# Performance work log

Measured on AMD Instinct MI355X. Metric: run time of the kernel, lower is better.

The kernel has to match this reference:

```python
import jax, jax.numpy as jnp
import numpy as np

B, N, L, D, H, DH = 1, 512, 256, 256, 8, 32  # batch, n_seqs, length, d_msa, heads, d_hidden
EPS = 1e-5


def setup_inputs() -> dict:
    key = jax.random.key(0)
    ks = jax.random.split(key, 3)
    msa = jax.random.normal(ks[0], (B, N, L, D), dtype=jnp.float32)
    # xavier-uniform-ish scale for (H*DH, D) linear weights
    lim = float(np.sqrt(6.0 / (D + H * DH)))
    Wq = jax.random.uniform(ks[1], (H * DH, D), minval=-lim, maxval=lim, dtype=jnp.float32)
    Wk = jax.random.uniform(ks[2], (H * DH, D), minval=-lim, maxval=lim, dtype=jnp.float32)
    return {
        "msa": msa,
        "Wq": Wq,
        "bq": jnp.zeros((H * DH,), jnp.float32),
        "Wk": Wk,
        "bk": jnp.zeros((H * DH,), jnp.float32),
        "ln_gamma": jnp.ones((D,), jnp.float32),
        "ln_beta": jnp.zeros((D,), jnp.float32),
        "stride": 0,
    }


def reference(msa, Wq, bq, Wk, bk, ln_gamma, ln_beta, stride):
    # stride only controls chunking in the original (no math effect); ignored.
    def ln(x):
        m = jnp.mean(x, axis=-1, keepdims=True)
        v = jnp.mean((x - m) ** 2, axis=-1, keepdims=True)
        return (x - m) * jax.lax.rsqrt(v + EPS) * ln_gamma + ln_beta

    scale = 1.0 / np.sqrt(DH)
    b, n, l = msa.shape[:3]
    # query from target (first) sequence: (B, L, H, DH)
    q = (ln(msa[:, 0]) @ Wq.T + bq).reshape(b, l, H, DH) * scale
    # keys from all sequences: (B, N, L, H, DH)
    k = (ln(msa) @ Wk.T + bk).reshape(b, n, l, H, DH)
    # attention logits over the sequence axis N: (B, N, L, H)
    logits = jnp.einsum("blhd,bnlhd->bnlh", q, k)
    attn = jax.nn.softmax(logits, axis=1)
    # dropout is identity in eval mode
    return attn[..., None]  # (B, N, L, H, 1)
```

## Files before the change

kernel.cpp:

```cpp
#include <hip/hip_runtime.h>
#include <hip/hip_bf16.h>
#include <cstdint>

#define LL 256
#define NN 512
#define DD 256
#define HH 8
#define EPSF 1e-5f
#define WGS 264
#define TS  264

typedef __attribute__((ext_vector_type(8))) __bf16 bf16x8;
typedef __attribute__((ext_vector_type(4))) __bf16 bf16x4;
typedef __attribute__((ext_vector_type(4))) float f32x4;

static __device__ __forceinline__ void lb_sync() {
    __builtin_amdgcn_sched_barrier(0);
    asm volatile("s_waitcnt lgkmcnt(0)" ::: "memory");
    __builtin_amdgcn_s_barrier();
    __builtin_amdgcn_sched_barrier(0);
}

static __device__ __forceinline__ void loadg(
    const float* __restrict__ msa, int l, int wave, int lane, int t, float4 (&buf)[16])
{
    #pragma unroll
    for (int r = 0; r < 16; ++r)
        buf[r] = *((const float4*)(msa + ((size_t)(t * 128 + wave * 16 + r) * LL + l) * DD) + lane);
}

static __device__ __forceinline__ void dswcvt(
    const float4 (&buf)[16], __bf16* tile, int wave, int lane)
{
    #pragma unroll
    for (int r = 0; r < 16; ++r) {
        float4 u = buf[r];
        bf16x4 b;
        b[0] = (__bf16)u.x; b[1] = (__bf16)u.y; b[2] = (__bf16)u.z; b[3] = (__bf16)u.w;
        *(bf16x4*)(tile + (wave * 16 + r) * TS + lane * 4) = b;
    }
}

static __device__ __forceinline__ void compute_t(
    int g, const __bf16* tile, const bf16x8 (&bfr)[8], int wave, int col, int kb,
    float* logits, float* sS, float* sQ)
{
    f32x4 ha = {0.f, 0.f, 0.f, 0.f}, ga = {0.f, 0.f, 0.f, 0.f};
    const __bf16* arow = tile + (wave * 16 + col) * TS;
    #pragma unroll
    for (int ks = 0; ks < 8; ++ks) {
        bf16x8 a = *(const bf16x8*)(arow + ks * 32 + kb * 8);
        ha = __builtin_amdgcn_mfma_f32_16x16x32_bf16(a, bfr[ks], ha, 0, 0, 0);
        ga = __builtin_amdgcn_mfma_f32_16x16x32_bf16(a, a,       ga, 0, 0, 0);
    }
    const int nb = g * 128 + wave * 16;
    #pragma unroll
    for (int i = 0; i < 4; ++i) {
        int n = nb + (kb << 2) + i;
        if (col < HH)       logits[col * NN + n] = ha[i];
        else if (col == HH) sS[n] = ha[i];
    }
    if (kb == (col >> 2)) sQ[nb + col] = ga[col & 3];
}

__global__ __launch_bounds__(512, 2) void k_fused(
    const float* __restrict__ msa, const float* __restrict__ Wq,
    const float* __restrict__ bq, const float* __restrict__ Wk,
    const float* __restrict__ gamma, const float* __restrict__ beta,
    float* __restrict__ out)
{
    const int l = blockIdx.x;
    const int tid = threadIdx.x, wave = tid >> 6, lane = tid & 63;
    const int col = lane & 15, kb = lane >> 4;

    __shared__ __align__(16) __bf16 tile[128 * TS];
    __shared__ __align__(16) __bf16 WgL[16 * WGS];
    __shared__ __align__(16) float logits[HH * NN];
    __shared__ __align__(16) float sS[NN];
    __shared__ __align__(16) float sQ[NN];
    __shared__ float lnx[DD];
    __shared__ float qv[DD];
    __shared__ float red[8];
    __shared__ float stats[16];
    __shared__ float Gs[HH];

    float4 P[16], Q[16];
    loadg(msa, l, wave, lane, 0, P);
    loadg(msa, l, wave, lane, 1, Q);

    {
        float x0 = (tid < DD) ? msa[(size_t)l * DD + tid] : 0.f;
        float s = x0, ss = x0 * x0;
        #pragma unroll
        for (int m = 32; m >= 1; m >>= 1) { s += __shfl_xor(s, m); ss += __shfl_xor(ss, m); }
        if (tid < DD && lane == 0) { red[wave * 2] = s; red[wave * 2 + 1] = ss; }
        lb_sync();
        if (tid < DD) {
            float sm = red[0] + red[2] + red[4] + red[6];
            float sq = red[1] + red[3] + red[5] + red[7];
            float mean = sm * (1.f / DD);
            float var  = sq * (1.f / DD) - mean * mean;
            float rs   = rsqrtf(var + EPSF);
            lnx[tid] = (x0 - mean) * rs * gamma[tid] + beta[tid];
        }
        lb_sync();
        const int r = tid & 255, hf = tid >> 8;
        float acc = 0.f;
        {
            const float4* wr = (const float4*)(Wq + (size_t)r * DD) + hf * 32;
            const float* lx = lnx + hf * 128;
            #pragma unroll 4
            for (int j = 0; j < 32; ++j) {
                float4 w4 = wr[j];
                acc += lx[4*j] * w4.x + lx[4*j+1] * w4.y + lx[4*j+2] * w4.z + lx[4*j+3] * w4.w;
            }
        }
        if (hf == 0) qv[r] = acc;
        lb_sync();
        if (hf == 1) qv[r] = (qv[r] + acc + bq[r]) * 0.17677669529663687f;
        lb_sync();
        const int c = tid & 255, h0 = (tid >> 8) * 4;
        const float gm = gamma[c];
        #pragma unroll
        for (int hi = 0; hi < 4; ++hi) {
            int h = h0 + hi;
            float a = 0.f;
            const float* wk = Wk + ((size_t)h * 32) * DD + c;
            #pragma unroll 8
            for (int d = 0; d < 32; ++d)
                a += qv[h * 32 + d] * wk[(size_t)d * DD];
            WgL[h * WGS + c] = (__bf16)(gm * a);
        }
        if (tid < DD) {
            WgL[8 * WGS + tid] = (__bf16)1.0f;
        } else {
            const int c2 = tid - 256;
            #pragma unroll
            for (int h = 9; h < 16; ++h) WgL[h * WGS + c2] = (__bf16)0.0f;
        }
        lb_sync();
        if (wave < HH) {
            float gsum = 0.f;
            #pragma unroll
            for (int i = 0; i < 4; ++i) gsum += (float)WgL[wave * WGS + lane * 4 + i];
            #pragma unroll
            for (int m = 32; m >= 1; m >>= 1) gsum += __shfl_xor(gsum, m);
            if (lane == 0) Gs[wave] = gsum;
        }
        lb_sync();
    }

    bf16x8 bfr[8];
    #pragma unroll
    for (int ks = 0; ks < 8; ++ks)
        bfr[ks] = *(const bf16x8*)&WgL[col * WGS + ks * 32 + kb * 8];

    dswcvt(P, tile, wave, lane);  loadg(msa, l, wave, lane, 2, P);  lb_sync();
    compute_t(0, tile, bfr, wave, col, kb, logits, sS, sQ);         lb_sync();
    dswcvt(Q, tile, wave, lane);  loadg(msa, l, wave, lane, 3, Q);  lb_sync();
    compute_t(1, tile, bfr, wave, col, kb, logits, sS, sQ);         lb_sync();
    dswcvt(P, tile, wave, lane);                                    lb_sync();
    compute_t(2, tile, bfr, wave, col, kb, logits, sS, sQ);         lb_sync();
    dswcvt(Q, tile, wave, lane);                                    lb_sync();
    compute_t(3, tile, bfr, wave, col, kb, logits, sS, sQ);         lb_sync();

    {
        const int h = wave;
        const float Gh = Gs[h];
        const float* lp = logits + h * NN;
        float4 ra = ((const float4*)lp)[lane * 2];
        float4 rb = ((const float4*)lp)[lane * 2 + 1];
        float4 sa = ((const float4*)sS)[lane * 2];
        float4 sb = ((const float4*)sS)[lane * 2 + 1];
        float4 qa = ((const float4*)sQ)[lane * 2];
        float4 qb = ((const float4*)sQ)[lane * 2 + 1];
        float raw[8] = {ra.x, ra.y, ra.z, ra.w, rb.x, rb.y, rb.z, rb.w};
        float sv[8]  = {sa.x, sa.y, sa.z, sa.w, sb.x, sb.y, sb.z, sb.w};
        float qv2[8] = {qa.x, qa.y, qa.z, qa.w, qb.x, qb.y, qb.z, qb.w};
        float adj[8];
        #pragma unroll
        for (int i = 0; i < 8; ++i) {
            float mean = sv[i] * (1.f / DD);
            float var  = qv2[i] * (1.f / DD) - mean * mean;
            float rs   = rsqrtf(var + EPSF);
            adj[i] = rs * (raw[i] - mean * Gh);
        }
        float mx = adj[0];
        #pragma unroll
        for (int i = 1; i < 8; ++i) mx = fmaxf(mx, adj[i]);
        #pragma unroll
        for (int m = 32; m >= 1; m >>= 1) mx = fmaxf(mx, __shfl_xor(mx, m));
        float sm = 0.f;
        #pragma unroll
        for (int i = 0; i < 8; ++i) sm += __expf(adj[i] - mx);
        #pragma unroll
        for (int m = 32; m >= 1; m >>= 1) sm += __shfl_xor(sm, m);
        if (lane == 0) { stats[wave] = mx; stats[8 + wave] = 1.f / sm; }
    }
    lb_sync();

    {
        const int n = tid;
        float s = sS[n], q2 = sQ[n];
        float mean = s * (1.f / DD);
        float var  = q2 * (1.f / DD) - mean * mean;
        float rs   = rsqrtf(var + EPSF);
        float o[8];
        #pragma unroll
        for (int h = 0; h < HH; ++h) {
            float adj = rs * (logits[h * NN + n] - mean * Gs[h]);
            o[h] = __expf(adj - stats[h]) * stats[8 + h];
        }
        float* op = out + (size_t)n * LL * HH + (size_t)l * HH;
        float4 p0 = {o[0], o[1], o[2], o[3]};
        float4 p1 = {o[4], o[5], o[6], o[7]};
        *(float4*)(op)     = p0;
        *(float4*)(op + 4) = p1;
    }
}

extern "C" void kernel_launch(void* const* d_in, const int* in_sizes, int n_in,
                              void* d_out, int out_size, void* d_ws, size_t ws_size,
                              hipStream_t stream) {
    (void)in_sizes; (void)n_in; (void)out_size; (void)d_ws; (void)ws_size;
    const float* msa   = (const float*)d_in[0];
    const float* Wq    = (const float*)d_in[1];
    const float* bq    = (const float*)d_in[2];
    const float* Wk    = (const float*)d_in[3];
    const float* gamma = (const float*)d_in[5];
    const float* beta  = (const float*)d_in[6];
    k_fused<<<dim3(LL), dim3(512), 0, stream>>>(msa, Wq, bq, Wk, gamma, beta, (float*)d_out);
}
```

Baseline: 44.77 us.

## Warp-specialize producer waves with async global-to-LDS double-buffered fp32 tiles

Replaces the register-staged load/convert/store pipeline with four producer waves that issue global_load_lds copies straight into two fp32 LDS tile buffers of 64 rows each. Four consumer waves convert to bf16 on the fly and run the MFMAs, with vmcnt waits and barriers handing off each buffer. To fit LDS, the WgL, lnx, qv and red scratch buffers are aliased into the logits buffer, and the Gs reduction moves after the bfr loads. The aim is to free the large register prefetch buffers and overlap memory traffic with compute. In exchange, half the waves no longer do MFMA, barriers run every step, and the larger LDS footprint limits residency to one block per CU.

```diff
diff --git a/kernel.cpp b/kernel.cpp
--- a/kernel.cpp
+++ b/kernel.cpp
@@ -8,10 +8,10 @@
 #define HH 8
 #define EPSF 1e-5f
 #define WGS 264
-#define TS  264
+#define TROWF 260
+#define TILEF (64 * TROWF)
 
 typedef __attribute__((ext_vector_type(8))) __bf16 bf16x8;
-typedef __attribute__((ext_vector_type(4))) __bf16 bf16x4;
 typedef __attribute__((ext_vector_type(4))) float f32x4;
 
 static __device__ __forceinline__ void lb_sync() {
@@ -21,49 +21,20 @@
     __builtin_amdgcn_sched_barrier(0);
 }
 
-static __device__ __forceinline__ void loadg(
-    const float* __restrict__ msa, int l, int wave, int lane, int t, float4 (&buf)[16])
+static __device__ __forceinline__ void stage16(
+    const float* __restrict__ msa, int l, int n0, float* ldsrow0, int lane)
 {
     #pragma unroll
-    for (int r = 0; r < 16; ++r)
-        buf[r] = *((const float4*)(msa + ((size_t)(t * 128 + wave * 16 + r) * LL + l) * DD) + lane);
-}
-
-static __device__ __forceinline__ void dswcvt(
-    const float4 (&buf)[16], __bf16* tile, int wave, int lane)
-{
-    #pragma unroll
-    for (int r = 0; r < 16; ++r) {
-        float4 u = buf[r];
-        bf16x4 b;
-        b[0] = (__bf16)u.x; b[1] = (__bf16)u.y; b[2] = (__bf16)u.z; b[3] = (__bf16)u.w;
-        *(bf16x4*)(tile + (wave * 16 + r) * TS + lane * 4) = b;
-    }
-}
-
-static __device__ __forceinline__ void compute_t(
-    int g, const __bf16* tile, const bf16x8 (&bfr)[8], int wave, int col, int kb,
-    float* logits, float* sS, float* sQ)
-{
-    f32x4 ha = {0.f, 0.f, 0.f, 0.f}, ga = {0.f, 0.f, 0.f, 0.f};
-    const __bf16* arow = tile + (wave * 16 + col) * TS;
-    #pragma unroll
-    for (int ks = 0; ks < 8; ++ks) {
-        bf16x8 a = *(const bf16x8*)(arow + ks * 32 + kb * 8);
-        ha = __builtin_amdgcn_mfma_f32_16x16x32_bf16(a, bfr[ks], ha, 0, 0, 0);
-        ga = __builtin_amdgcn_mfma_f32_16x16x32_bf16(a, a,       ga, 0, 0, 0);
-    }
-    const int nb = g * 128 + wave * 16;
-    #pragma unroll
-    for (int i = 0; i < 4; ++i) {
-        int n = nb + (kb << 2) + i;
-        if (col < HH)       logits[col * NN + n] = ha[i];
-        else if (col == HH) sS[n] = ha[i];
-    }
-    if (kb == (col >> 2)) sQ[nb + col] = ga[col & 3];
-}
-
-__global__ __launch_bounds__(512, 2) void k_fused(
+    for (int i = 0; i < 16; ++i) {
+        const float* g = msa + ((size_t)(n0 + i) * LL + l) * DD + lane * 4;
+        __builtin_amdgcn_global_load_lds(
+            (const __attribute__((address_space(1))) void*)g,
+            (__attribute__((address_space(3))) void*)(ldsrow0 + (size_t)i * TROWF),
+            16, 0, 0);
+    }
+}
+
+__global__ __launch_bounds__(512) void k_fused(
     const float* __restrict__ msa, const float* __restrict__ Wq,
     const float* __restrict__ bq, const float* __restrict__ Wk,
     const float* __restrict__ gamma, const float* __restrict__ beta,
@@ -73,20 +44,24 @@
     const int tid = threadIdx.x, wave = tid >> 6, lane = tid & 63;
     const int col = lane & 15, kb = lane >> 4;
 
-    __shared__ __align__(16) __bf16 tile[128 * TS];
-    __shared__ __align__(16) __bf16 WgL[16 * WGS];
-    __shared__ __align__(16) float logits[HH * NN];
+    __shared__ __align__(16) float TileF[2 * TILEF];
+    __shared__ __align__(16) float logitsBuf[HH * NN];
     __shared__ __align__(16) float sS[NN];
     __shared__ __align__(16) float sQ[NN];
-    __shared__ float lnx[DD];
-    __shared__ float qv[DD];
-    __shared__ float red[8];
     __shared__ float stats[16];
     __shared__ float Gs[HH];
 
-    float4 P[16], Q[16];
-    loadg(msa, l, wave, lane, 0, P);
-    loadg(msa, l, wave, lane, 1, Q);
+    __bf16* WgL = (__bf16*)logitsBuf;
+    float*  lnx = logitsBuf + 2112;
+    float*  qv  = lnx + 256;
+    float*  red = qv + 256;
+    float*  logits = logitsBuf;
+
+    if (wave >= 4) {
+        const int pid = wave - 4;
+        stage16(msa, l, 0 * 64 + pid * 16, TileF + 0 * TILEF + pid * 16 * TROWF, lane);
+        stage16(msa, l, 1 * 64 + pid * 16, TileF + 1 * TILEF + pid * 16 * TROWF, lane);
+    }
 
     {
         float x0 = (tid < DD) ? msa[(size_t)l * DD + tid] : 0.f;
@@ -139,30 +114,59 @@
             for (int h = 9; h < 16; ++h) WgL[h * WGS + c2] = (__bf16)0.0f;
         }
         lb_sync();
-        if (wave < HH) {
-            float gsum = 0.f;
-            #pragma unroll
-            for (int i = 0; i < 4; ++i) gsum += (float)WgL[wave * WGS + lane * 4 + i];
-            #pragma unroll
-            for (int m = 32; m >= 1; m >>= 1) gsum += __shfl_xor(gsum, m);
-            if (lane == 0) Gs[wave] = gsum;
-        }
-        lb_sync();
     }
 
     bf16x8 bfr[8];
     #pragma unroll
     for (int ks = 0; ks < 8; ++ks)
         bfr[ks] = *(const bf16x8*)&WgL[col * WGS + ks * 32 + kb * 8];
-
-    dswcvt(P, tile, wave, lane);  loadg(msa, l, wave, lane, 2, P);  lb_sync();
-    compute_t(0, tile, bfr, wave, col, kb, logits, sS, sQ);         lb_sync();
-    dswcvt(Q, tile, wave, lane);  loadg(msa, l, wave, lane, 3, Q);  lb_sync();
-    compute_t(1, tile, bfr, wave, col, kb, logits, sS, sQ);         lb_sync();
-    dswcvt(P, tile, wave, lane);                                    lb_sync();
-    compute_t(2, tile, bfr, wave, col, kb, logits, sS, sQ);         lb_sync();
-    dswcvt(Q, tile, wave, lane);                                    lb_sync();
-    compute_t(3, tile, bfr, wave, col, kb, logits, sS, sQ);         lb_sync();
+    {
+        float gsum = 0.f;
+        #pragma unroll
+        for (int i = 0; i < 4; ++i) gsum += (float)WgL[wave * WGS + lane * 4 + i];
+        #pragma unroll
+        for (int m = 32; m >= 1; m >>= 1) gsum += __shfl_xor(gsum, m);
+        if (lane == 0) Gs[wave] = gsum;
+    }
+    lb_sync();
+
+    const f32x4 z = {0.f, 0.f, 0.f, 0.f};
+    #pragma unroll 1
+    for (int t = 0; t < 8; ++t) {
+        const int buf = t & 1;
+        if (wave >= 4) {
+            if (t == 7) asm volatile("s_waitcnt vmcnt(0)" ::: "memory");
+            else        asm volatile("s_waitcnt vmcnt(16)" ::: "memory");
+        }
+        lb_sync();
+        if (wave < 4) {
+            f32x4 ha = z, ga = z;
+            const float* tb = TileF + buf * TILEF + (wave * 16 + col) * TROWF;
+            #pragma unroll
+            for (int ks = 0; ks < 8; ++ks) {
+                float4 u = *(const float4*)(tb + ks * 32 + kb * 8);
+                float4 v = *(const float4*)(tb + ks * 32 + kb * 8 + 4);
+                bf16x8 a;
+                a[0] = (__bf16)u.x; a[1] = (__bf16)u.y; a[2] = (__bf16)u.z; a[3] = (__bf16)u.w;
+                a[4] = (__bf16)v.x; a[5] = (__bf16)v.y; a[6] = (__bf16)v.z; a[7] = (__bf16)v.w;
+                ha = __builtin_amdgcn_mfma_f32_16x16x32_bf16(a, bfr[ks], ha, 0, 0, 0);
+                ga = __builtin_amdgcn_mfma_f32_16x16x32_bf16(a, a,       ga, 0, 0, 0);
+            }
+            const int nb = t * 64 + wave * 16;
+            #pragma unroll
+            for (int i = 0; i < 4; ++i) {
+                int n = nb + (kb << 2) + i;
+                if (col < HH)       logits[col * NN + n] = ha[i];
+                else if (col == HH) sS[n] = ha[i];
+            }
+            if (kb == (col >> 2)) sQ[nb + col] = ga[col & 3];
+        }
+        lb_sync();
+        if (wave >= 4 && t + 2 < 8) {
+            const int pid = wave - 4;
+            stage16(msa, l, (t + 2) * 64 + pid * 16, TileF + buf * TILEF + pid * 16 * TROWF, lane);
+        }
+    }
 
     {
         const int h = wave;
```

Result: no change. 45.60 us (+1.8%).
